# Kernel tuning notes

Hardware: AMD Instinct MI355X
Metric: run time of the kernel (lower is better)

Reference implementation:

```python
import jax, jax.numpy as jnp
import numpy as np

# Dimensions: B graphs of NPG nodes each (equal sizes -> padding == reshape, exact)
B, NPG, DIN, H, E, DOUT, K_ORDER = 8, 4096, 128, 4, 262144, 128, 4
BETA = 0.5
N = B * NPG


def setup_inputs() -> dict:
    key = jax.random.key(0)
    k = jax.random.split(key, 12)
    s = 1.0 / np.sqrt(DIN)
    so = 1.0 / np.sqrt(H * DIN)
    x = jax.random.normal(k[0], (N, DIN), jnp.float32)
    Wq_w = jax.random.normal(k[1], (H * DIN, DIN), jnp.float32) * s
    Wq_b = jax.random.normal(k[2], (H * DIN,), jnp.float32) * 0.01
    Wk_w = jax.random.normal(k[3], (H * DIN, DIN), jnp.float32) * s
    Wk_b = jax.random.normal(k[4], (H * DIN,), jnp.float32) * 0.01
    Wo_w = jax.random.normal(k[5], (DOUT, H * DIN), jnp.float32) * so
    Wo_b = jax.random.normal(k[6], (DOUT,), jnp.float32) * 0.01
    # edges constrained within graphs (faithful to per-graph data)
    g = jax.random.randint(k[7], (E,), 0, B)
    row = g * NPG + jax.random.randint(k[8], (E,), 0, NPG)
    col = g * NPG + jax.random.randint(k[9], (E,), 0, NPG)
    edge_index = jnp.stack([row, col]).astype(jnp.int32)
    n_nodes = jnp.full((B,), NPG, jnp.int32)
    return {"x": x, "Wq_w": Wq_w, "Wq_b": Wq_b, "Wk_w": Wk_w, "Wk_b": Wk_b,
            "Wo_w": Wo_w, "Wo_b": Wo_b, "edge_index": edge_index, "n_nodes": n_nodes}


def _gcn(x, row, col):
    # x: [N,H,D]; symmetric-normalized message passing via segment sums
    deg = jax.ops.segment_sum(jnp.ones(row.shape[0], x.dtype), row, num_segments=N)
    safe = jnp.where(deg > 0, deg, 1.0)
    dis = jnp.where(deg > 0, safe ** -0.5, 0.0)
    w = (dis[row] * dis[col])[:, None, None]
    return jax.ops.segment_sum(x[col] * w, row, num_segments=N)


def _attn(qs, ks, v, n_f):
    # linear attention: out_i = (q_i . sum_j k_j v_j^T + sum_j v_j) / (q_i . sum_j k_j + n)
    q4 = qs.reshape(B, NPG, H, DIN)
    k4 = ks.reshape(B, NPG, H, DIN)
    v4 = v.reshape(B, NPG, H, DIN)
    kv = jnp.einsum('bnhd,bnhe->bhde', k4, v4)          # [B,H,D,D]
    ksum = k4.sum(axis=1)                                # [B,H,D]
    vsum = v4.sum(axis=1)                                # [B,H,D]
    num = jnp.einsum('bnhd,bhde->bnhe', q4, kv) + vsum[:, None]
    den = jnp.einsum('bnhd,bhd->bnh', q4, ksum) + n_f[:, None, None]
    return (num / den[..., None]).reshape(N, H, DIN)


def reference(x, Wq_w, Wq_b, Wk_w, Wk_b, Wo_w, Wo_b, edge_index, n_nodes):
    row, col = edge_index[0], edge_index[1]
    q = (x @ Wq_w.T + Wq_b).reshape(N, H, DIN)
    k = (x @ Wk_w.T + Wk_b).reshape(N, H, DIN)
    qs = q / jnp.linalg.norm(q, axis=2, keepdims=True)
    ks = k / jnp.linalg.norm(k, axis=2, keepdims=True)
    n_f = n_nodes.astype(x.dtype)
    xh = jnp.broadcast_to(x[:, None, :], (N, H, DIN))    # repeat over heads
    acc = xh
    cur = xh
    for _ in range(K_ORDER):
        cur = BETA * _gcn(cur, row, col) + (1.0 - BETA) * _attn(qs, ks, cur, n_f)
        acc = acc + cur
    xo = acc.reshape(N, H * DIN)
    return (xo @ Wo_w.T + Wo_b) / H
```

## Files before the change

kernel.cpp:

```cpp
#include <hip/hip_runtime.h>
#include <hip/hip_bf16.h>
#include <stdint.h>

typedef __hip_bfloat16 bf16;

#define BATCH  8
#define NPG    4096
#define DIN    128
#define NH     4
#define NEDGE  262144
#define DOUTF  128
#define KORDER 4
#define NTOT   (BATCH*NPG)
#define HD     (NH*DIN)

typedef __attribute__((ext_vector_type(8))) short short8;
typedef __attribute__((ext_vector_type(4))) float f32x4;

static __device__ __forceinline__ float b2f(bf16 v) { return __bfloat162float(v); }
static __device__ __forceinline__ float u2f(unsigned short u) {
    union { float f; unsigned int i; } c; c.i = ((unsigned int)u) << 16; return c.f;
}
static __device__ __forceinline__ unsigned short f2u(float f) {
    bf16 hb = __float2bfloat16(f);
    return *(unsigned short*)&hb;
}

__global__ void zero_kernel(uint4* p, int n) {
    int i = blockIdx.x * 256 + threadIdx.x;
    if (i < n) p[i] = uint4{0u, 0u, 0u, 0u};
}

__global__ void cvtbf_kernel(const float* __restrict__ in, bf16* __restrict__ out, int n) {
    int i = (blockIdx.x * 256 + threadIdx.x) * 8;
    if (i < n) {
        float4 a = *(const float4*)(in + i);
        float4 b = *(const float4*)(in + i + 4);
        unsigned short u[8] = { f2u(a.x), f2u(a.y), f2u(a.z), f2u(a.w),
                                f2u(b.x), f2u(b.y), f2u(b.z), f2u(b.w) };
        *(uint4*)(out + i) = *(uint4*)u;
    }
}

__global__ __launch_bounds__(256) void proj_mfma_kernel(const bf16* __restrict__ xbf,
                                                        const bf16* __restrict__ Wbf,
                                                        const float* __restrict__ bias,
                                                        bf16* __restrict__ outp,
                                                        bf16* __restrict__ outT) {
    __shared__ __align__(16) short t1[32][520];
    int n0 = blockIdx.x * 32;
    int tid = threadIdx.x;
    int lane = tid & 63, wc = tid >> 6;
    int l15 = lane & 15, quad = lane >> 4;

    f32x4 acc[2][8];
    #pragma unroll
    for (int i = 0; i < 2; i++)
        #pragma unroll
        for (int j = 0; j < 8; j++) acc[i][j] = f32x4{0.f, 0.f, 0.f, 0.f};

    #pragma unroll
    for (int ks = 0; ks < 4; ks++) {
        int kk = ks * 32 + quad * 8;
        short8 af[2];
        #pragma unroll
        for (int ti = 0; ti < 2; ti++)
            af[ti] = *(const short8*)(xbf + (size_t)(n0 + ti * 16 + l15) * DIN + kk);
        #pragma unroll
        for (int tj = 0; tj < 8; tj++) {
            short8 bfr = *(const short8*)(Wbf + (size_t)(wc * 128 + tj * 16 + l15) * DIN + kk);
            acc[0][tj] = __builtin_amdgcn_mfma_f32_16x16x32_bf16(af[0], bfr, acc[0][tj], 0, 0, 0);
            acc[1][tj] = __builtin_amdgcn_mfma_f32_16x16x32_bf16(af[1], bfr, acc[1][tj], 0, 0, 0);
        }
    }

    float bias_v[8];
    #pragma unroll
    for (int tj = 0; tj < 8; tj++) bias_v[tj] = bias[wc * 128 + tj * 16 + l15];

    #pragma unroll
    for (int ti = 0; ti < 2; ti++) {
        #pragma unroll
        for (int r = 0; r < 4; r++) {
            float s = 0.f;
            #pragma unroll
            for (int tj = 0; tj < 8; tj++) {
                float v = acc[ti][tj][r] + bias_v[tj];
                acc[ti][tj][r] = v;
                s += v * v;
            }
            s += __shfl_xor(s, 1); s += __shfl_xor(s, 2);
            s += __shfl_xor(s, 4); s += __shfl_xor(s, 8);
            float rs = rsqrtf(s);
            int node = ti * 16 + quad * 4 + r;
            #pragma unroll
            for (int tj = 0; tj < 8; tj++)
                t1[node][wc * 128 + tj * 16 + l15] = (short)f2u(acc[ti][tj][r] * rs);
        }
    }
    __syncthreads();

    if (outp) {
        #pragma unroll
        for (int u = 0; u < 8; u++) {
            int unit = u * 256 + tid;
            int nl = unit >> 6, fp = (unit & 63) * 8;
            *(uint4*)(outp + (size_t)(n0 + nl) * HD + fp) = *(uint4*)&t1[nl][fp];
        }
    }
    if (outT) {
        int b = n0 >> 12, nl0 = n0 & 4095;
        #pragma unroll
        for (int u = 0; u < 8; u++) {
            int unit = u * 256 + tid;
            int f = unit >> 2, np = (unit & 3) * 8;
            unsigned short arr[8];
            #pragma unroll
            for (int j = 0; j < 8; j++) arr[j] = (unsigned short)t1[np + j][f];
            *(uint4*)(outT + ((size_t)b * HD + f) * NPG + nl0 + np) = *(uint4*)arr;
        }
    }
}

__global__ void deg_kernel(const int* __restrict__ row, int* __restrict__ deg) {
    int e = blockIdx.x * 256 + threadIdx.x;
    if (e < NEDGE) atomicAdd(&deg[row[e]], 1);
}

__global__ void dis_kernel(const int* __restrict__ deg, float* __restrict__ dis) {
    int i = blockIdx.x * 256 + threadIdx.x;
    if (i < NTOT) {
        int d = deg[i];
        dis[i] = d > 0 ? rsqrtf((float)d) : 0.f;
    }
}

__global__ __launch_bounds__(1024) void scan1_kernel(const int* __restrict__ deg,
                                                     int* __restrict__ row_ptr, int* __restrict__ bsum) {
    __shared__ int buf[1024];
    int g = blockIdx.x, t = threadIdx.x;
    int v = deg[g * 1024 + t];
    buf[t] = v;
    __syncthreads();
    for (int off = 1; off < 1024; off <<= 1) {
        int add = (t >= off) ? buf[t - off] : 0;
        __syncthreads();
        buf[t] += add;
        __syncthreads();
    }
    row_ptr[g * 1024 + t] = buf[t] - v;
    if (t == 1023) bsum[g] = buf[1023];
}

__global__ void scan2_kernel(const int* __restrict__ bsum, int* __restrict__ boff, int* __restrict__ row_ptr) {
    int run = 0;
    for (int g = 0; g < 32; g++) { boff[g] = run; run += bsum[g]; }
    row_ptr[NTOT] = run;
}

__global__ __launch_bounds__(1024) void scan3_kernel(int* __restrict__ row_ptr, const int* __restrict__ boff) {
    row_ptr[blockIdx.x * 1024 + threadIdx.x] += boff[blockIdx.x];
}

__global__ void scatter_kernel(const int* __restrict__ row, const int* __restrict__ col,
                               const int* __restrict__ row_ptr, int* __restrict__ fill,
                               const float* __restrict__ dis,
                               uint2* __restrict__ ecw) {
    int e = blockIdx.x * 256 + threadIdx.x;
    if (e < NEDGE) {
        int r = row[e], c = col[e];
        int pos = row_ptr[r] + atomicAdd(&fill[r], 1);
        ecw[pos] = uint2{(unsigned)c, __float_as_uint(dis[c])};
    }
}

__global__ __launch_bounds__(256) void rowsum_kernel(const bf16* __restrict__ T, float* __restrict__ out) {
    int row = blockIdx.x * 4 + (threadIdx.x >> 6);
    int lane = threadIdx.x & 63;
    const ushort4* p = (const ushort4*)(T + (size_t)row * NPG);
    float s = 0.f;
    #pragma unroll
    for (int wv = 0; wv < 16; wv++) {
        ushort4 u = p[lane + wv * 64];
        s += u2f(u.x) + u2f(u.y) + u2f(u.z) + u2f(u.w);
    }
    for (int off = 32; off > 0; off >>= 1) s += __shfl_down(s, off);
    if (lane == 0) out[row] = s;
}

__global__ __launch_bounds__(256) void colsum_kernel(const bf16* __restrict__ xbf, float* __restrict__ vsum) {
    __shared__ float buf[256];
    int b = blockIdx.x >> 3, sl = blockIdx.x & 7;
    int t = threadIdx.x;
    int d = t & 127, half = t >> 7;
    const unsigned short* p = (const unsigned short*)xbf + ((size_t)b * NPG + sl * 512 + half * 256) * DIN + d;
    float s = 0.f;
    for (int r = 0; r < 256; r++) s += u2f(p[(size_t)r * DIN]);
    buf[t] = s;
    __syncthreads();
    if (half == 0) {
        float tot = buf[d] + buf[d + 128];
        #pragma unroll
        for (int h = 0; h < NH; h++) atomicAdd(&vsum[b * HD + h * DIN + d], tot);
    }
}

__global__ __launch_bounds__(256) void den_kernel(const bf16* __restrict__ qs, const float* __restrict__ ksum,
                                                  const int* __restrict__ n_nodes, float* __restrict__ rden) {
    int n = blockIdx.x;
    int b = n >> 12;
    int w = threadIdx.x >> 6, lane = threadIdx.x & 63;
    int base = w * DIN;
    float p = b2f(qs[(size_t)n * HD + base + lane])      * ksum[b * HD + base + lane]
            + b2f(qs[(size_t)n * HD + base + 64 + lane]) * ksum[b * HD + base + 64 + lane];
    for (int off = 32; off > 0; off >>= 1) p += __shfl_down(p, off);
    if (lane == 0) rden[n * NH + w] = 1.0f / (p + (float)n_nodes[b]);
}

#define KVSPLIT 8
__global__ __launch_bounds__(512, 1) void kv_mfma_kernel(const bf16* __restrict__ ksT,
                                                         const bf16* __restrict__ vsrc,
                                                         int vld, int vhm,
                                                         float* __restrict__ partial) {
    __shared__ __align__(16) short kshT[128][72];
    __shared__ __align__(16) short vshT[128][72];
    int id = blockIdx.x;
    int b = id & 7;
    int u = id >> 3;
    int h = u >> 3;
    int s = u & 7;
    int bh = b * 4 + h;
    int blk = bh * KVSPLIT + s;
    int tid = threadIdx.x;
    int lane = tid & 63;
    int w = tid >> 6;
    int wr = w >> 1, wc = w & 1;
    int d0w = wr * 32, e0w = wc * 64;
    int l15 = lane & 15, quad = lane >> 4;

    f32x4 acc[2][4];
    #pragma unroll
    for (int i = 0; i < 2; i++)
        #pragma unroll
        for (int j = 0; j < 4; j++) acc[i][j] = f32x4{0.f, 0.f, 0.f, 0.f};

    const uint4* kg = (const uint4*)(ksT + ((size_t)bh * 128) * NPG);
    const bf16* vg = vsrc + (size_t)h * vhm;
    int n0 = s * (NPG / KVSPLIT);

    for (int c = 0; c < 8; c++) {
        int nb = n0 + c * 64;
        #pragma unroll
        for (int uu = 0; uu < 2; uu++) {
            int unit = uu * 512 + tid;
            int row = unit >> 3;
            int part = unit & 7;
            uint4 kd = kg[row * (NPG / 8) + (nb >> 3) + part];
            *(uint4*)&kshT[row][part * 8] = kd;
            int nl = unit >> 4;
            int fg = unit & 15;
            uint4 vd = *(const uint4*)(vg + (size_t)(b * NPG + nb + nl) * vld + fg * 8);
            unsigned short* sv = (unsigned short*)&vd;
            int ncol = nl ^ ((fg & 7) << 3);
            #pragma unroll
            for (int j = 0; j < 8; j++) vshT[fg * 8 + j][ncol] = (short)sv[j];
        }
        __syncthreads();
        #pragma unroll
        for (int kkstep = 0; kkstep < 2; kkstep++) {
            int kk = kkstep * 32 + quad * 8;
            short8 af[2], bfr[4];
            #pragma unroll
            for (int ti = 0; ti < 2; ti++)
                af[ti] = *(const short8*)&kshT[d0w + ti * 16 + l15][kk];
            #pragma unroll
            for (int tj = 0; tj < 4; tj++) {
                int e = e0w + tj * 16 + l15;
                bfr[tj] = *(const short8*)&vshT[e][kk ^ (((e >> 3) & 7) << 3)];
            }
            #pragma unroll
            for (int ti = 0; ti < 2; ti++)
                #pragma unroll
                for (int tj = 0; tj < 4; tj++)
                    acc[ti][tj] = __builtin_amdgcn_mfma_f32_16x16x32_bf16(af[ti], bfr[tj], acc[ti][tj], 0, 0, 0);
        }
        __syncthreads();
    }
    float* p = partial + (size_t)blk * (128 * 128);
    #pragma unroll
    for (int ti = 0; ti < 2; ti++)
        #pragma unroll
        for (int tj = 0; tj < 4; tj++)
            #pragma unroll
            for (int r = 0; r < 4; r++) {
                int row = d0w + ti * 16 + quad * 4 + r;
                int col = e0w + tj * 16 + l15;
                p[row * 128 + col] = acc[ti][tj][r];
            }
}

__global__ __launch_bounds__(256) void kvredB_kernel(const float* __restrict__ partial, bf16* __restrict__ kvB) {
    __shared__ __align__(16) short t[16][136];
    int blk = blockIdx.x;
    int bh = blk >> 3;
    int e0 = (blk & 7) * 16;
    int tid = threadIdx.x;
    int el = tid & 15;
    int dc = tid >> 4;
    const float* p = partial + (size_t)bh * (KVSPLIT * 16384);
    #pragma unroll
    for (int j = 0; j < 8; j++) {
        int d = dc * 8 + j;
        int idx = d * 128 + e0 + el;
        float s = 0.f;
        #pragma unroll
        for (int sl = 0; sl < KVSPLIT; sl++) s += p[sl * 16384 + idx];
        t[el][d] = (short)f2u(s);
    }
    __syncthreads();
    int e = tid >> 4, dp = (tid & 15) * 8;
    *(uint4*)((unsigned short*)kvB + (size_t)bh * 16384 + (e0 + e) * 128 + dp) = *(uint4*)&t[e][dp];
}

static __device__ __forceinline__ void acc8(float* g, uint4 v, float w) {
    unsigned short* sv = (unsigned short*)&v;
    #pragma unroll
    for (int k = 0; k < 8; k++) g[k] += w * u2f(sv[k]);
}

#define EMAX 1536
__global__ __launch_bounds__(512, 2) void gcn_attn_kernel(const bf16* __restrict__ qs,
                                                          const bf16* __restrict__ kvB,
                                                          const bf16* __restrict__ gsrc,
                                                          int gld, int ghm,
                                                          const int* __restrict__ row_ptr,
                                                          const uint2* __restrict__ ecw,
                                                          const float* __restrict__ dis,
                                                          const float* __restrict__ vsum,
                                                          const float* __restrict__ rden,
                                                          bf16* __restrict__ curN,
                                                          float* __restrict__ vsumN) {
    __shared__ __align__(16) short t1[128][136];
    __shared__ __align__(8) uint2 est[EMAX];
    int id = blockIdx.x;
    int b = id & 7;
    int u = id >> 3;
    int h = u >> 5;
    int m = u & 31;
    int bh = b * 4 + h;
    int n0 = b * NPG + m * 128;
    int tid = threadIdx.x;
    int lane = tid & 63, w = tid >> 6;
    int wr = w >> 1, wc = w & 1;
    int e0w = wc * 64;
    int l15 = lane & 15, quad = lane >> 4;

    int ebase = row_ptr[n0];
    int ecnt = row_ptr[n0 + 128] - ebase;
    int scnt = ecnt < EMAX ? ecnt : EMAX;
    for (int i = tid; i < scnt; i += 512) est[i] = ecw[ebase + i];
    __syncthreads();

    {
        int nl = tid >> 2;
        int sub = tid & 3;
        int n = n0 + nl;
        int start = row_ptr[n] - ebase;
        int end   = row_ptr[n + 1] - ebase;
        int lend  = end < scnt ? end : scnt;
        float g[32];
        #pragma unroll
        for (int i = 0; i < 32; i++) g[i] = 0.f;
        const bf16* gbase = gsrc + (size_t)h * ghm + sub * 32;

        int cA = 0, cB = 0; float wA = 0.f, wB = 0.f;
        if (start < lend)     { uint2 p = est[start];     cA = (int)p.x; wA = __uint_as_float(p.y); }
        if (start + 1 < lend) { uint2 p = est[start + 1]; cB = (int)p.x; wB = __uint_as_float(p.y); }
        uint4 vA0, vA1, vA2, vA3, vB0, vB1, vB2, vB3;
        {
            const uint4* p = (const uint4*)(gbase + (size_t)cA * gld);
            vA0 = p[0]; vA1 = p[1]; vA2 = p[2]; vA3 = p[3];
        }
        {
            const uint4* p = (const uint4*)(gbase + (size_t)cB * gld);
            vB0 = p[0]; vB1 = p[1]; vB2 = p[2]; vB3 = p[3];
        }
        for (int j = start; j < lend; j += 2) {
            int cC = 0, cD = 0; float wC = 0.f, wD = 0.f;
            if (j + 2 < lend) { uint2 p = est[j + 2]; cC = (int)p.x; wC = __uint_as_float(p.y); }
            if (j + 3 < lend) { uint2 p = est[j + 3]; cD = (int)p.x; wD = __uint_as_float(p.y); }
            acc8(g +  0, vA0, wA); acc8(g +  8, vA1, wA);
            acc8(g + 16, vA2, wA); acc8(g + 24, vA3, wA);
            {
                const uint4* p = (const uint4*)(gbase + (size_t)cC * gld);
                vA0 = p[0]; vA1 = p[1]; vA2 = p[2]; vA3 = p[3];
            }
            acc8(g +  0, vB0, wB); acc8(g +  8, vB1, wB);
            acc8(g + 16, vB2, wB); acc8(g + 24, vB3, wB);
            {
                const uint4* p = (const uint4*)(gbase + (size_t)cD * gld);
                vB0 = p[0]; vB1 = p[1]; vB2 = p[2]; vB3 = p[3];
            }
            wA = wC; wB = wD;
        }
        int fstart = start > lend ? start : lend;
        for (int j = fstart; j < end; j++) {
            uint2 pe = ecw[ebase + j];
            int c = (int)pe.x; float ww = __uint_as_float(pe.y);
            const uint4* p = (const uint4*)(gbase + (size_t)c * gld);
            acc8(g +  0, p[0], ww); acc8(g +  8, p[1], ww);
            acc8(g + 16, p[2], ww); acc8(g + 24, p[3], ww);
        }

        float dn = dis[n];
        int sw = (nl >> 3) & 7;
        #pragma unroll
        for (int q = 0; q < 4; q++) {
            unsigned short arr[8];
            #pragma unroll
            for (int k = 0; k < 8; k++) arr[k] = f2u(g[q * 8 + k] * dn);
            int fb = (sub * 4 + q) ^ sw;
            *(uint4*)&t1[nl][fb * 8] = *(uint4*)arr;
        }
    }

    f32x4 acc[2][4];
    #pragma unroll
    for (int i = 0; i < 2; i++)
        #pragma unroll
        for (int j = 0; j < 4; j++) acc[i][j] = f32x4{0.f, 0.f, 0.f, 0.f};

    const bf16* Aq = qs + (size_t)n0 * HD + h * DIN;
    const unsigned short* Bk = (const unsigned short*)kvB + (size_t)bh * 16384;
    #pragma unroll
    for (int ks = 0; ks < 4; ks++) {
        int kk = ks * 32 + quad * 8;
        short8 af[2], bfr[4];
        #pragma unroll
        for (int ti = 0; ti < 2; ti++)
            af[ti] = *(const short8*)(Aq + (size_t)(wr * 32 + ti * 16 + l15) * HD + kk);
        #pragma unroll
        for (int tj = 0; tj < 4; tj++)
            bfr[tj] = *(const short8*)(Bk + (e0w + tj * 16 + l15) * 128 + kk);
        #pragma unroll
        for (int ti = 0; ti < 2; ti++)
            #pragma unroll
            for (int tj = 0; tj < 4; tj++)
                acc[ti][tj] = __builtin_amdgcn_mfma_f32_16x16x32_bf16(af[ti], bfr[tj], acc[ti][tj], 0, 0, 0);
    }
    __syncthreads();

    #pragma unroll
    for (int tj = 0; tj < 4; tj++) {
        int el = e0w + tj * 16 + l15;
        float vs = vsum[b * HD + h * DIN + el];
        float cs = 0.f;
        #pragma unroll
        for (int ti = 0; ti < 2; ti++) {
            int nlb = wr * 32 + ti * 16 + quad * 4;
            #pragma unroll
            for (int r = 0; r < 4; r++) {
                int nl = nlb + r;
                int sw = (nl >> 3) & 7;
                int pc = (((el >> 3) ^ sw) * 8) | (el & 7);
                float attnv = (acc[ti][tj][r] + vs) * rden[(size_t)(n0 + nl) * NH + h];
                float g = u2f((unsigned short)t1[nl][pc]);
                float val = 0.5f * g + 0.5f * attnv;
                t1[nl][pc] = (short)f2u(val);
                cs += val;
            }
        }
        cs += __shfl_xor(cs, 16);
        cs += __shfl_xor(cs, 32);
        if (quad == 0) atomicAdd(&vsumN[b * HD + h * DIN + el], cs);
    }
    __syncthreads();

    {
        bf16* dstn = curN + (size_t)n0 * HD + h * DIN;
        #pragma unroll
        for (int uu = 0; uu < 4; uu++) {
            int unit = uu * 512 + tid;
            int nl = unit >> 4, fb = unit & 15;
            int sw = (nl >> 3) & 7;
            uint4 v = *(uint4*)&t1[nl][(fb ^ sw) * 8];
            *(uint4*)(dstn + (size_t)nl * HD + fb * 8) = v;
        }
    }
}

__global__ __launch_bounds__(512) void out_mfma_kernel(const bf16* __restrict__ xbf,
                                                       const bf16* __restrict__ c1,
                                                       const bf16* __restrict__ c2,
                                                       const bf16* __restrict__ c3,
                                                       const bf16* __restrict__ c4,
                                                       const bf16* __restrict__ Wobf,
                                                       const float* __restrict__ Wo_b,
                                                       float* __restrict__ out) {
    int n0 = blockIdx.x * 128;
    int tid = threadIdx.x;
    int lane = tid & 63, w = tid >> 6;
    int wr = w >> 1, wc = w & 1;
    int l15 = lane & 15, quad = lane >> 4;

    f32x4 acc[2][4];
    #pragma unroll
    for (int i = 0; i < 2; i++)
        #pragma unroll
        for (int j = 0; j < 4; j++) acc[i][j] = f32x4{0.f, 0.f, 0.f, 0.f};

    for (int ks = 0; ks < 16; ks++) {
        int kk = ks * 32 + quad * 8;
        int d = kk & 127;
        short8 af[2], bfr[4];
        #pragma unroll
        for (int ti = 0; ti < 2; ti++) {
            int row = n0 + wr * 32 + ti * 16 + l15;
            uint4 vx = *(const uint4*)(xbf + (size_t)row * DIN + d);
            uint4 v1 = *(const uint4*)(c1 + (size_t)row * HD + kk);
            uint4 v2 = *(const uint4*)(c2 + (size_t)row * HD + kk);
            uint4 v3 = *(const uint4*)(c3 + (size_t)row * HD + kk);
            uint4 v4 = *(const uint4*)(c4 + (size_t)row * HD + kk);
            unsigned short* px = (unsigned short*)&vx;
            unsigned short* p1 = (unsigned short*)&v1;
            unsigned short* p2 = (unsigned short*)&v2;
            unsigned short* p3 = (unsigned short*)&v3;
            unsigned short* p4 = (unsigned short*)&v4;
            unsigned short o[8];
            #pragma unroll
            for (int j = 0; j < 8; j++)
                o[j] = f2u(u2f(px[j]) + u2f(p1[j]) + u2f(p2[j]) + u2f(p3[j]) + u2f(p4[j]));
            af[ti] = *(short8*)o;
        }
        #pragma unroll
        for (int tj = 0; tj < 4; tj++)
            bfr[tj] = *(const short8*)(Wobf + (size_t)(wc * 64 + tj * 16 + l15) * HD + kk);
        #pragma unroll
        for (int ti = 0; ti < 2; ti++)
            #pragma unroll
            for (int tj = 0; tj < 4; tj++)
                acc[ti][tj] = __builtin_amdgcn_mfma_f32_16x16x32_bf16(af[ti], bfr[tj], acc[ti][tj], 0, 0, 0);
    }

    #pragma unroll
    for (int tj = 0; tj < 4; tj++) {
        int col = wc * 64 + tj * 16 + l15;
        float bv = Wo_b[col];
        #pragma unroll
        for (int ti = 0; ti < 2; ti++) {
            int rowb = wr * 32 + ti * 16 + quad * 4;
            #pragma unroll
            for (int r = 0; r < 4; r++)
                out[(size_t)(n0 + rowb + r) * DOUTF + col] = (acc[ti][tj][r] + bv) * 0.25f;
        }
    }
}

extern "C" void kernel_launch(void* const* d_in, const int* in_sizes, int n_in,
                              void* d_out, int out_size, void* d_ws, size_t ws_size,
                              hipStream_t stream) {
    const float* x     = (const float*)d_in[0];
    const float* Wq_w  = (const float*)d_in[1];
    const float* Wq_b  = (const float*)d_in[2];
    const float* Wk_w  = (const float*)d_in[3];
    const float* Wk_b  = (const float*)d_in[4];
    const float* Wo_w  = (const float*)d_in[5];
    const float* Wo_b  = (const float*)d_in[6];
    const int*   edge  = (const int*)d_in[7];
    const int*   n_nod = (const int*)d_in[8];
    float* out = (float*)d_out;
    const int* erow = edge;
    const int* ecol = edge + NEDGE;

    char* w = (char*)d_ws;
    auto alloc = [&](size_t bytes) -> char* {
        char* p = w;
        w += (bytes + 255) & ~(size_t)255;
        return p;
    };
    bf16*  qs      = (bf16*) alloc((size_t)NTOT * HD * 2);
    bf16*  ksT     = (bf16*) alloc((size_t)NTOT * HD * 2);
    bf16*  cur1    = (bf16*) alloc((size_t)NTOT * HD * 2);
    bf16*  cur2    = (bf16*) alloc((size_t)NTOT * HD * 2);
    bf16*  cur3    = (bf16*) alloc((size_t)NTOT * HD * 2);
    bf16*  cur4    = (bf16*) alloc((size_t)NTOT * HD * 2);
    bf16*  xbf     = (bf16*) alloc((size_t)NTOT * DIN * 2);
    float* partial = (float*)alloc((size_t)32 * KVSPLIT * 16384 * 4);
    bf16*  kvB     = (bf16*) alloc((size_t)32 * 16384 * 2);
    bf16*  Wobf    = (bf16*) alloc(DOUTF * HD * 2);
    int*   degfill = (int*)  alloc(2 * NTOT * 4);
    float* dis     = (float*)alloc(NTOT * 4);
    int*   row_ptr = (int*)  alloc((NTOT + 1) * 4);
    uint2* ecw     = (uint2*)alloc((size_t)NEDGE * 8);
    float* ksum    = (float*)alloc(BATCH * HD * 4);
    float* vsumA   = (float*)alloc(BATCH * HD * 4);
    float* vsumB   = (float*)alloc(BATCH * HD * 4);
    float* rden    = (float*)alloc((size_t)NTOT * NH * 4);
    int*   bsum    = (int*)  alloc(32 * 4);
    int*   boff    = (int*)  alloc(32 * 4);
    int* deg  = degfill;
    int* fill = degfill + NTOT;
    bf16* Wqbf = (bf16*)partial;
    bf16* Wkbf = Wqbf + (size_t)HD * DIN;

    zero_kernel<<<64, 256, 0, stream>>>((uint4*)degfill, 2 * NTOT / 4);

    cvtbf_kernel<<<NTOT * DIN / 8 / 256, 256, 0, stream>>>(x, xbf, NTOT * DIN);
    cvtbf_kernel<<<HD * DIN / 8 / 256, 256, 0, stream>>>(Wq_w, Wqbf, HD * DIN);
    cvtbf_kernel<<<HD * DIN / 8 / 256, 256, 0, stream>>>(Wk_w, Wkbf, HD * DIN);
    cvtbf_kernel<<<DOUTF * HD / 8 / 256, 256, 0, stream>>>(Wo_w, Wobf, DOUTF * HD);

    proj_mfma_kernel<<<NTOT / 32, 256, 0, stream>>>(xbf, Wqbf, Wq_b, qs, (bf16*)nullptr);
    proj_mfma_kernel<<<NTOT / 32, 256, 0, stream>>>(xbf, Wkbf, Wk_b, (bf16*)nullptr, ksT);

    deg_kernel<<<NEDGE / 256, 256, 0, stream>>>(erow, deg);
    dis_kernel<<<NTOT / 256, 256, 0, stream>>>(deg, dis);
    scan1_kernel<<<32, 1024, 0, stream>>>(deg, row_ptr, bsum);
    scan2_kernel<<<1, 1, 0, stream>>>(bsum, boff, row_ptr);
    scan3_kernel<<<32, 1024, 0, stream>>>(row_ptr, boff);
    scatter_kernel<<<NEDGE / 256, 256, 0, stream>>>(erow, ecol, row_ptr, fill, dis, ecw);

    rowsum_kernel<<<BATCH * HD / 4, 256, 0, stream>>>(ksT, ksum);
    den_kernel<<<NTOT, 256, 0, stream>>>(qs, ksum, n_nod, rden);

    zero_kernel<<<4, 256, 0, stream>>>((uint4*)vsumA, BATCH * HD / 4);
    colsum_kernel<<<64, 256, 0, stream>>>(xbf, vsumA);

    bf16* curs[4] = { cur1, cur2, cur3, cur4 };
    float* vs = vsumA;
    float* vsN = vsumB;
    for (int it = 0; it < KORDER; it++) {
        const bf16* src = (it == 0) ? xbf : curs[it - 1];
        int ld = (it == 0) ? DIN : HD;
        int hm = (it == 0) ? 0 : DIN;
        kv_mfma_kernel<<<32 * KVSPLIT, 512, 0, stream>>>(ksT, src, ld, hm, partial);
        kvredB_kernel<<<256, 256, 0, stream>>>(partial, kvB);
        zero_kernel<<<4, 256, 0, stream>>>((uint4*)vsN, BATCH * HD / 4);
        gcn_attn_kernel<<<32 * 32, 512, 0, stream>>>(qs, kvB, src, ld, hm, row_ptr, ecw, dis,
                                                     vs, rden, curs[it], vsN);
        float* tf = vs; vs = vsN; vsN = tf;
    }

    out_mfma_kernel<<<NTOT / 128, 512, 0, stream>>>(xbf, cur1, cur2, cur3, cur4, Wobf, Wo_b, out);

    (void)in_sizes; (void)n_in; (void)out_size; (void)ws_size;
}
```

Baseline: 579.3 us.

## Raise kv split count, tighten launch bounds, restage output GEMM via LDS

Doubles the node split in the KV outer-product kernel and raises its occupancy hint. Raises the occupancy hint on the fused GCN/attention kernel. Rewrites the output projection to sum the five bf16 inputs once into a shared-memory tile over 32 rows, then run MFMA from LDS with smaller blocks. The tighter launch bounds may force register spills, and the larger KV split doubles the partial buffer traffic and reduction work.

```diff
diff --git a/kernel.cpp b/kernel.cpp
--- a/kernel.cpp
+++ b/kernel.cpp
@@ -217,8 +217,8 @@
     if (lane == 0) rden[n * NH + w] = 1.0f / (p + (float)n_nodes[b]);
 }
 
-#define KVSPLIT 8
-__global__ __launch_bounds__(512, 1) void kv_mfma_kernel(const bf16* __restrict__ ksT,
+#define KVSPLIT 16
+__global__ __launch_bounds__(512, 4) void kv_mfma_kernel(const bf16* __restrict__ ksT,
                                                          const bf16* __restrict__ vsrc,
                                                          int vld, int vhm,
                                                          float* __restrict__ partial) {
@@ -227,8 +227,8 @@
     int id = blockIdx.x;
     int b = id & 7;
     int u = id >> 3;
-    int h = u >> 3;
-    int s = u & 7;
+    int h = u >> 4;
+    int s = u & 15;
     int bh = b * 4 + h;
     int blk = bh * KVSPLIT + s;
     int tid = threadIdx.x;
@@ -248,7 +248,7 @@
     const bf16* vg = vsrc + (size_t)h * vhm;
     int n0 = s * (NPG / KVSPLIT);
 
-    for (int c = 0; c < 8; c++) {
+    for (int c = 0; c < NPG / KVSPLIT / 64; c++) {
         int nb = n0 + c * 64;
         #pragma unroll
         for (int uu = 0; uu < 2; uu++) {
@@ -329,7 +329,7 @@
 }
 
 #define EMAX 1536
-__global__ __launch_bounds__(512, 2) void gcn_attn_kernel(const bf16* __restrict__ qs,
+__global__ __launch_bounds__(512, 6) void gcn_attn_kernel(const bf16* __restrict__ qs,
                                                           const bf16* __restrict__ kvB,
                                                           const bf16* __restrict__ gsrc,
                                                           int gld, int ghm,
@@ -489,66 +489,74 @@
     }
 }
 
-__global__ __launch_bounds__(512) void out_mfma_kernel(const bf16* __restrict__ xbf,
-                                                       const bf16* __restrict__ c1,
-                                                       const bf16* __restrict__ c2,
-                                                       const bf16* __restrict__ c3,
-                                                       const bf16* __restrict__ c4,
-                                                       const bf16* __restrict__ Wobf,
-                                                       const float* __restrict__ Wo_b,
-                                                       float* __restrict__ out) {
-    int n0 = blockIdx.x * 128;
+__global__ __launch_bounds__(256, 4) void out_mfma_kernel(const bf16* __restrict__ xbf,
+                                                          const bf16* __restrict__ c1,
+                                                          const bf16* __restrict__ c2,
+                                                          const bf16* __restrict__ c3,
+                                                          const bf16* __restrict__ c4,
+                                                          const bf16* __restrict__ Wobf,
+                                                          const float* __restrict__ Wo_b,
+                                                          float* __restrict__ out) {
+    __shared__ __align__(16) short ash[32][520];
+    int n0 = blockIdx.x * 32;
     int tid = threadIdx.x;
     int lane = tid & 63, w = tid >> 6;
-    int wr = w >> 1, wc = w & 1;
     int l15 = lane & 15, quad = lane >> 4;
 
-    f32x4 acc[2][4];
+    #pragma unroll 4
+    for (int uu = 0; uu < 8; uu++) {
+        int unit = uu * 256 + tid;
+        int row = unit >> 6, cg = unit & 63;
+        int col = cg * 8;
+        size_t rbase = (size_t)(n0 + row);
+        uint4 vx = *(const uint4*)(xbf + rbase * DIN + (col & 127));
+        uint4 v1 = *(const uint4*)(c1 + rbase * HD + col);
+        uint4 v2 = *(const uint4*)(c2 + rbase * HD + col);
+        uint4 v3 = *(const uint4*)(c3 + rbase * HD + col);
+        uint4 v4 = *(const uint4*)(c4 + rbase * HD + col);
+        unsigned short* px = (unsigned short*)&vx;
+        unsigned short* p1 = (unsigned short*)&v1;
+        unsigned short* p2 = (unsigned short*)&v2;
+        unsigned short* p3 = (unsigned short*)&v3;
+        unsigned short* p4 = (unsigned short*)&v4;
+        unsigned short o[8];
+        #pragma unroll
+        for (int j = 0; j < 8; j++)
+            o[j] = f2u(u2f(px[j]) + u2f(p1[j]) + u2f(p2[j]) + u2f(p3[j]) + u2f(p4[j]));
+        *(uint4*)&ash[row][col] = *(uint4*)o;
+    }
+    __syncthreads();
+
+    f32x4 acc[2][2];
     #pragma unroll
     for (int i = 0; i < 2; i++)
         #pragma unroll
-        for (int j = 0; j < 4; j++) acc[i][j] = f32x4{0.f, 0.f, 0.f, 0.f};
-
+        for (int j = 0; j < 2; j++) acc[i][j] = f32x4{0.f, 0.f, 0.f, 0.f};
+
+    #pragma unroll
     for (int ks = 0; ks < 16; ks++) {
         int kk = ks * 32 + quad * 8;
-        int d = kk & 127;
-        short8 af[2], bfr[4];
+        short8 af[2], bfr[2];
+        #pragma unroll
+        for (int ti = 0; ti < 2; ti++)
+            af[ti] = *(const short8*)&ash[ti * 16 + l15][kk];
+        #pragma unroll
+        for (int tj = 0; tj < 2; tj++)
+            bfr[tj] = *(const short8*)(Wobf + (size_t)(w * 32 + tj * 16 + l15) * HD + kk);
+        #pragma unroll
+        for (int ti = 0; ti < 2; ti++)
+            #pragma unroll
+            for (int tj = 0; tj < 2; tj++)
+                acc[ti][tj] = __builtin_amdgcn_mfma_f32_16x16x32_bf16(af[ti], bfr[tj], acc[ti][tj], 0, 0, 0);
+    }
+
+    #pragma unroll
+    for (int tj = 0; tj < 2; tj++) {
+        int col = w * 32 + tj * 16 + l15;
+        float bv = Wo_b[col];
         #pragma unroll
         for (int ti = 0; ti < 2; ti++) {
-            int row = n0 + wr * 32 + ti * 16 + l15;
-            uint4 vx = *(const uint4*)(xbf + (size_t)row * DIN + d);
-            uint4 v1 = *(const uint4*)(c1 + (size_t)row * HD + kk);
-            uint4 v2 = *(const uint4*)(c2 + (size_t)row * HD + kk);
-            uint4 v3 = *(const uint4*)(c3 + (size_t)row * HD + kk);
-            uint4 v4 = *(const uint4*)(c4 + (size_t)row * HD + kk);
-            unsigned short* px = (unsigned short*)&vx;
-            unsigned short* p1 = (unsigned short*)&v1;
-            unsigned short* p2 = (unsigned short*)&v2;
-            unsigned short* p3 = (unsigned short*)&v3;
-            unsigned short* p4 = (unsigned short*)&v4;
-            unsigned short o[8];
-            #pragma unroll
-            for (int j = 0; j < 8; j++)
-                o[j] = f2u(u2f(px[j]) + u2f(p1[j]) + u2f(p2[j]) + u2f(p3[j]) + u2f(p4[j]));
-            af[ti] = *(short8*)o;
-        }
-        #pragma unroll
-        for (int tj = 0; tj < 4; tj++)
-            bfr[tj] = *(const short8*)(Wobf + (size_t)(wc * 64 + tj * 16 + l15) * HD + kk);
-        #pragma unroll
-        for (int ti = 0; ti < 2; ti++)
-            #pragma unroll
-            for (int tj = 0; tj < 4; tj++)
-                acc[ti][tj] = __builtin_amdgcn_mfma_f32_16x16x32_bf16(af[ti], bfr[tj], acc[ti][tj], 0, 0, 0);
-    }
-
-    #pragma unroll
-    for (int tj = 0; tj < 4; tj++) {
-        int col = wc * 64 + tj * 16 + l15;
-        float bv = Wo_b[col];
-        #pragma unroll
-        for (int ti = 0; ti < 2; ti++) {
-            int rowb = wr * 32 + ti * 16 + quad * 4;
+            int rowb = ti * 16 + quad * 4;
             #pragma unroll
             for (int r = 0; r < 4; r++)
                 out[(size_t)(n0 + rowb + r) * DOUTF + col] = (acc[ti][tj][r] + bv) * 0.25f;
@@ -641,7 +649,7 @@
         float* tf = vs; vs = vsN; vsN = tf;
     }
 
-    out_mfma_kernel<<<NTOT / 128, 512, 0, stream>>>(xbf, cur1, cur2, cur3, cur4, Wobf, Wo_b, out);
+    out_mfma_kernel<<<NTOT / 32, 256, 0, stream>>>(xbf, cur1, cur2, cur3, cur4, Wobf, Wo_b, out);
 
     (void)in_sizes; (void)n_in; (void)out_size; (void)ws_size;
 }
```

Result: slower. 1.010 ms (+74.4%).
